# Optimization experiments

Measured on AMD Instinct MI355X. Metric: run time of the kernel, lower is better.

Reference implementation:

```python
import jax, jax.numpy as jnp
import numpy as np

B, L, V, E, H, DH, M, NL, BS, NR = 4, 2048, 32000, 512, 8, 64, 2048, 4, 64, 3
NEG = -1e9


def _sinusoidal_pe(length, dim):
    # LRA common_layers sinusoidal init: first half sin, second half cos.
    pos = np.arange(length, dtype=np.float32)[:, None]
    half = dim // 2
    div = np.exp(np.arange(half, dtype=np.float32) * -(np.log(10000.0) / half))
    pe = np.zeros((length, dim), np.float32)
    pe[:, :half] = np.sin(pos * div)
    pe[:, half:2 * half] = np.cos(pos * div)
    return jnp.asarray(pe)


def _bigbird_block_mask(seq_len, block_size, num_rand, seed):
    # BigBird sparsity at block granularity: window(3-band) + global(first/last
    # block rows & cols) + num_rand random blocks per row (connectivity_seed).
    nb = seq_len // block_size
    m = np.zeros((nb, nb), dtype=bool)
    for i in range(nb):
        for d in (-1, 0, 1):
            j = i + d
            if 0 <= j < nb:
                m[i, j] = True
    m[0, :] = True
    m[-1, :] = True
    m[:, 0] = True
    m[:, -1] = True
    rng = np.random.RandomState(seed)
    for i in range(1, nb - 1):
        avoid = {0, nb - 1, i - 1, i, i + 1}
        cand = np.array([j for j in range(nb) if j not in avoid])
        pick = rng.permutation(cand)[:num_rand]
        m[i, pick] = True
    return jnp.asarray(np.kron(m, np.ones((block_size, block_size), dtype=bool)))


_SPARSE_MASKS = [_bigbird_block_mask(L, BS, NR, lyr) for lyr in range(NL)]  # [L,L] bool per layer
_PE = _sinusoidal_pe(L, E)


def _ln(x, scale, bias, eps=1e-6):
    mu = jnp.mean(x, axis=-1, keepdims=True)
    var = jnp.mean(jnp.square(x - mu), axis=-1, keepdims=True)
    return (x - mu) * jax.lax.rsqrt(var + eps) * scale + bias


def setup_inputs() -> dict:
    key = jax.random.key(0)
    ks = jax.random.split(key, 12)
    s_qkv = 1.0 / np.sqrt(E)
    s_mlp = 1.0 / np.sqrt(E)
    return {
        "tokens": jax.random.randint(ks[0], (B, L), 0, V, dtype=jnp.int32),
        "embed": jax.random.normal(ks[1], (V, E), jnp.float32),
        "ln1_s": jnp.ones((NL, E), jnp.float32),
        "ln1_b": jnp.zeros((NL, E), jnp.float32),
        "wq": jax.random.normal(ks[2], (NL, E, H, DH), jnp.float32) * s_qkv,
        "wk": jax.random.normal(ks[3], (NL, E, H, DH), jnp.float32) * s_qkv,
        "wv": jax.random.normal(ks[4], (NL, E, H, DH), jnp.float32) * s_qkv,
        "wo": jax.random.normal(ks[5], (NL, H, DH, E), jnp.float32) * s_qkv,
        "ln2_s": jnp.ones((NL, E), jnp.float32),
        "ln2_b": jnp.zeros((NL, E), jnp.float32),
        "w1": jax.random.normal(ks[6], (NL, E, M), jnp.float32) * s_mlp,
        "b1": jnp.zeros((NL, M), jnp.float32),
        "w2": jax.random.normal(ks[7], (NL, M, E), jnp.float32) * (1.0 / np.sqrt(M)),
        "b2": jnp.zeros((NL, E), jnp.float32),
        "lnf_s": jnp.ones((E,), jnp.float32),
        "lnf_b": jnp.zeros((E,), jnp.float32),
    }


def reference(tokens, embed, ln1_s, ln1_b, wq, wk, wv, wo,
              ln2_s, ln2_b, w1, b1, w2, b2, lnf_s, lnf_b):
    pad = tokens > 0                                  # [B,L]
    x = embed[tokens] + _PE[None]                     # [B,L,E]
    scale = 1.0 / jnp.sqrt(jnp.asarray(DH, x.dtype))
    for lyr in range(NL):
        y = _ln(x, ln1_s[lyr], ln1_b[lyr])
        q = jnp.einsum("ble,ehd->blhd", y, wq[lyr]) * scale
        k = jnp.einsum("ble,ehd->blhd", y, wk[lyr])
        v = jnp.einsum("ble,ehd->blhd", y, wv[lyr])
        scores = jnp.einsum("blhd,bmhd->bhlm", q, k)  # [B,H,L,L]
        mask = (_SPARSE_MASKS[lyr][None, None]
                & pad[:, None, :, None] & pad[:, None, None, :])
        probs = jax.nn.softmax(jnp.where(mask, scores, NEG), axis=-1)
        o = jnp.einsum("bhlm,bmhd->blhd", probs, v)
        x = x + jnp.einsum("blhd,hde->ble", o, wo[lyr])
        y = _ln(x, ln2_s[lyr], ln2_b[lyr])
        h = jax.nn.gelu(jnp.einsum("ble,em->blm", y, w1[lyr]) + b1[lyr])
        x = x + jnp.einsum("blm,me->ble", h, w2[lyr]) + b2[lyr]
    return _ln(x, lnf_s, lnf_b)
```

## Files before the change

kernel.cpp:

```cpp
#include <hip/hip_runtime.h>
#include <hip/hip_bf16.h>
#include <cmath>
#include <cstdint>
#include <cstddef>

#define B_   4
#define L_   2048
#define E_   512
#define H_   8
#define DH_  64
#define M_   2048
#define NL_  4
#define NB_  32
#define BS_  64
#define CH_  12

typedef short bf16x8 __attribute__((ext_vector_type(8)));
typedef short bf16x4 __attribute__((ext_vector_type(4)));
typedef float f32x4 __attribute__((ext_vector_type(4)));

__device__ __forceinline__ short f2bf(float f) {
    union { __hip_bfloat16 h; short s; } u;
    u.h = __float2bfloat16(f);
    return u.s;
}
__device__ __forceinline__ float bf2f(short s) {
    union { short s; __hip_bfloat16 h; } u;
    u.s = s;
    return __bfloat162float(u.h);
}

struct MaskTable { unsigned m[NL_][NB_]; };
struct CxMT { unsigned key[624]; int pos; };

constexpr unsigned cx_next(CxMT& st) {
    if (st.pos >= 624) {
        for (int i = 0; i < 624; ++i) {
            unsigned y = (st.key[i] & 0x80000000u) | (st.key[(i + 1) % 624] & 0x7fffffffu);
            st.key[i] = st.key[(i + 397) % 624] ^ (y >> 1) ^ ((y & 1u) ? 0x9908b0dfu : 0u);
        }
        st.pos = 0;
    }
    unsigned y = st.key[st.pos++];
    y ^= y >> 11;
    y ^= (y << 7) & 0x9d2c5680u;
    y ^= (y << 15) & 0xefc60000u;
    y ^= y >> 18;
    return y;
}
constexpr unsigned cx_interval(CxMT& st, unsigned maxv) {
    if (maxv == 0u) return 0u;
    unsigned mask = maxv;
    mask |= mask >> 1; mask |= mask >> 2; mask |= mask >> 4;
    mask |= mask >> 8; mask |= mask >> 16;
    unsigned v = cx_next(st) & mask;
    while (v > maxv) v = cx_next(st) & mask;
    return v;
}
constexpr MaskTable compute_masks() {
    MaskTable T{};
    for (int lyr = 0; lyr < NL_; ++lyr) {
        unsigned m[NB_] = {};
        for (int i = 0; i < NB_; ++i) {
            unsigned w = 1u << i;
            if (i > 0) w |= 1u << (i - 1);
            if (i < NB_ - 1) w |= 1u << (i + 1);
            w |= 1u | (1u << (NB_ - 1));
            m[i] = w;
        }
        m[0] = 0xffffffffu;
        m[NB_ - 1] = 0xffffffffu;
        CxMT st{};
        unsigned s = (unsigned)lyr;
        for (int i = 0; i < 624; ++i) {
            st.key[i] = s;
            s = 1812433253u * (s ^ (s >> 30)) + (unsigned)i + 1u;
        }
        st.pos = 624;
        for (int i = 1; i < NB_ - 1; ++i) {
            int cand[NB_] = {};
            int n = 0;
            for (int j = 0; j < NB_; ++j) {
                if (j == 0 || j == NB_ - 1 || j == i - 1 || j == i || j == i + 1) continue;
                cand[n++] = j;
            }
            for (int kk = n - 1; kk >= 1; --kk) {
                int jj = (int)cx_interval(st, (unsigned)kk);
                int tmp = cand[kk]; cand[kk] = cand[jj]; cand[jj] = tmp;
            }
            m[i] |= (1u << cand[0]) | (1u << cand[1]) | (1u << cand[2]);
        }
        for (int i = 0; i < NB_; ++i) T.m[lyr][i] = m[i];
    }
    return T;
}

struct WorkTable {
    int n_items[NL_];
    int n_cmb[NL_];
    unsigned char itm_qb[NL_][40];
    unsigned char itm_j0[NL_][40];
    unsigned char itm_jn[NL_][40];
    unsigned char itm_slot[NL_][40];
    unsigned char cmb_qb[NL_][8];
    unsigned char cmb_slot0[NL_][8];
    unsigned char cmb_nch[NL_][8];
    unsigned char jlist[NL_][NB_][NB_];
};

constexpr WorkTable compute_work() {
    WorkTable T{};
    MaskTable M = compute_masks();
    for (int lyr = 0; lyr < NL_; ++lyr) {
        int items = 0, slots = 0, ncmb = 0;
        for (int qb = 0; qb < NB_; ++qb) {
            int cnt = 0;
            for (int j = 0; j < NB_; ++j)
                if ((M.m[lyr][qb] >> j) & 1u)
                    T.jlist[lyr][qb][cnt++] = (unsigned char)j;
            int nch = (cnt + CH_ - 1) / CH_;
            if (nch == 1) {
                T.itm_qb[lyr][items] = (unsigned char)qb;
                T.itm_j0[lyr][items] = 0;
                T.itm_jn[lyr][items] = (unsigned char)cnt;
                T.itm_slot[lyr][items] = 0xFF;
                items++;
            } else {
                T.cmb_qb[lyr][ncmb] = (unsigned char)qb;
                T.cmb_slot0[lyr][ncmb] = (unsigned char)slots;
                T.cmb_nch[lyr][ncmb] = (unsigned char)nch;
                ncmb++;
                int base = cnt / nch, rem = cnt % nch, off = 0;
                for (int c = 0; c < nch; ++c) {
                    int cl = base + (c < rem ? 1 : 0);
                    T.itm_qb[lyr][items] = (unsigned char)qb;
                    T.itm_j0[lyr][items] = (unsigned char)off;
                    T.itm_jn[lyr][items] = (unsigned char)cl;
                    T.itm_slot[lyr][items] = (unsigned char)slots;
                    items++; slots++; off += cl;
                }
            }
        }
        T.n_items[lyr] = items;
        T.n_cmb[lyr] = ncmb;
    }
    return T;
}

static constexpr WorkTable WT_HOST = compute_work();
__constant__ WorkTable g_wt = compute_work();

__global__ __launch_bounds__(256) void embed_kernel(const int* __restrict__ tokens,
                                                    const float* __restrict__ embed,
                                                    float* __restrict__ x) {
    int idx = blockIdx.x * 256 + threadIdx.x;
    int l = idx >> 6;
    int e0 = (idx & 63) * 8;
    float pe[8];
    #pragma unroll
    for (int j = 0; j < 8; ++j) {
        int e = e0 + j;
        int jj = e & 255;
        float div = expf((float)jj * -0.03597789207717895f);
        float arg = (float)l * div;
        pe[j] = (e < 256) ? sinf(arg) : cosf(arg);
    }
    #pragma unroll
    for (int b = 0; b < B_; ++b) {
        int tok = tokens[b * L_ + l];
        const float* em = embed + (size_t)tok * E_ + e0;
        f32x4 v0 = *(const f32x4*)em;
        f32x4 v1 = *(const f32x4*)(em + 4);
        #pragma unroll
        for (int j = 0; j < 4; ++j) { v0[j] += pe[j]; v1[j] += pe[4 + j]; }
        float* xo = x + ((size_t)(b * L_ + l)) * E_ + e0;
        *(f32x4*)xo = v0;
        *(f32x4*)(xo + 4) = v1;
    }
}

template<int OUTBF>
__global__ __launch_bounds__(256) void ln_kernel(const float* __restrict__ x,
                                                 const float* __restrict__ gamma,
                                                 const float* __restrict__ beta,
                                                 void* __restrict__ yout) {
    int t = threadIdx.x;
    int lane = t & 63;
    int row = blockIdx.x * 4 + (t >> 6);
    const float* xr = x + (size_t)row * E_ + lane * 8;
    f32x4 a0 = *(const f32x4*)xr;
    f32x4 a1 = *(const f32x4*)(xr + 4);
    float s = a0[0] + a0[1] + a0[2] + a0[3] + a1[0] + a1[1] + a1[2] + a1[3];
    #pragma unroll
    for (int off = 1; off < 64; off <<= 1) s += __shfl_xor(s, off, 64);
    float mu = s * (1.0f / E_);
    float q = 0.0f;
    #pragma unroll
    for (int j = 0; j < 4; ++j) { float d = a0[j] - mu; q += d * d; }
    #pragma unroll
    for (int j = 0; j < 4; ++j) { float d = a1[j] - mu; q += d * d; }
    #pragma unroll
    for (int off = 1; off < 64; off <<= 1) q += __shfl_xor(q, off, 64);
    float rstd = rsqrtf(q * (1.0f / E_) + 1e-6f);
    f32x4 g0 = *(const f32x4*)(gamma + lane * 8);
    f32x4 g1 = *(const f32x4*)(gamma + lane * 8 + 4);
    f32x4 b0 = *(const f32x4*)(beta + lane * 8);
    f32x4 b1 = *(const f32x4*)(beta + lane * 8 + 4);
    float o[8];
    #pragma unroll
    for (int j = 0; j < 4; ++j) o[j] = (a0[j] - mu) * rstd * g0[j] + b0[j];
    #pragma unroll
    for (int j = 0; j < 4; ++j) o[4 + j] = (a1[j] - mu) * rstd * g1[j] + b1[j];
    if (OUTBF) {
        bf16x8 pk;
        #pragma unroll
        for (int j = 0; j < 8; ++j) pk[j] = f2bf(o[j]);
        *(bf16x8*)((short*)yout + (size_t)row * E_ + lane * 8) = pk;
    } else {
        float* yr = (float*)yout + (size_t)row * E_ + lane * 8;
        *(f32x4*)yr = f32x4{o[0], o[1], o[2], o[3]};
        *(f32x4*)(yr + 4) = f32x4{o[4], o[5], o[6], o[7]};
    }
}

__global__ __launch_bounds__(256) void convT_kernel(const float* __restrict__ W,
                                                    short* __restrict__ Wt,
                                                    int K, int N,
                                                    size_t wStride, size_t wtStride,
                                                    float scale) {
    __shared__ float Ts[64][65];
    const float* Wl = W + blockIdx.z * wStride;
    short* Wtl = Wt + blockIdx.z * wtStride;
    int n0 = blockIdx.x * 64, k0 = blockIdx.y * 64;
    int t = threadIdx.x;
    int c = t & 63, r0 = t >> 6;
    #pragma unroll
    for (int i = 0; i < 16; ++i) {
        int r = r0 * 16 + i;
        Ts[r][c] = Wl[(size_t)(k0 + r) * N + n0 + c] * scale;
    }
    __syncthreads();
    #pragma unroll
    for (int i = 0; i < 16; ++i) {
        int r = r0 * 16 + i;
        Wtl[(size_t)(n0 + r) * K + k0 + c] = f2bf(Ts[c][r]);
    }
}

__device__ __forceinline__ float gelu_tanh(float x) {
    float u = x * (1.5957691216057308f + 0.07135480122394604f * x * x);
    return x / (1.0f + __expf(-u));
}

template<int BM, int BN, int WR, int WC, int ACT, int OUTBF>
__global__ __launch_bounds__(256) void mgemm_kernel(const short* __restrict__ A,
                                                    const short* __restrict__ Bt,
                                                    const float* __restrict__ bias,
                                                    const float* __restrict__ res,
                                                    void* __restrict__ Cout,
                                                    int M, int N, int K) {
    constexpr int FM = BM / WR / 16;
    constexpr int FN = BN / WC / 16;
    constexpr int ASZ = BM * 64;
    constexpr int BSZ = BN * 64;
    constexpr int PAD = 8;
    constexpr int CW = BN + PAD;
    static_assert((size_t)(OUTBF ? BM * CW * 2 : BM * CW * 4) <= (size_t)2 * (ASZ + BSZ) * 2,
                  "epilogue stage must fit in dbuf LDS");
    __shared__ __align__(16) short smem[2 * (ASZ + BSZ)];

    int t = threadIdx.x;
    int w = t >> 6, l = t & 63;
    int l15 = l & 15, lg = l >> 4;
    int wr = w / WC, wc = w % WC;
    int rowbase = wr * (BM / WR), colbase = wc * (BN / WC);
    int brow = blockIdx.y * BM, bcol = blockIdx.x * BN;
    int swz = ((l & 7) ^ (l >> 3)) * 8;
    int lrow = l >> 3;
    f32x4 acc[FM][FN] = {};

    const int nt = K >> 6;

    auto stage = [&](int buf, int k0) {
        short* Ad = smem + buf * ASZ;
        short* Bd = smem + 2 * ASZ + buf * BSZ;
        #pragma unroll
        for (int it = 0; it < BM / 32; ++it) {
            int row8 = (it * 4 + w) * 8;
            const short* ga = A + (size_t)(brow + row8 + lrow) * K + k0 + swz;
            __builtin_amdgcn_global_load_lds(
                (const __attribute__((address_space(1))) unsigned int*)ga,
                (__attribute__((address_space(3))) unsigned int*)(Ad + row8 * 64),
                16, 0, 0);
        }
        #pragma unroll
        for (int it = 0; it < BN / 32; ++it) {
            int row8 = (it * 4 + w) * 8;
            const short* gb = Bt + (size_t)(bcol + row8 + lrow) * K + k0 + swz;
            __builtin_amdgcn_global_load_lds(
                (const __attribute__((address_space(1))) unsigned int*)gb,
                (__attribute__((address_space(3))) unsigned int*)(Bd + row8 * 64),
                16, 0, 0);
        }
    };

    stage(0, 0);
    asm volatile("s_waitcnt vmcnt(0)" ::: "memory");
    __builtin_amdgcn_s_barrier();

    int cur = 0;
    for (int kt = 0; kt < nt; ++kt) {
        if (kt + 1 < nt) stage(cur ^ 1, (kt + 1) << 6);
        const short* Ar = smem + cur * ASZ;
        const short* Br = smem + 2 * ASZ + cur * BSZ;
        #pragma unroll
        for (int kk = 0; kk < 64; kk += 32) {
            bf16x8 af[FM], bfr[FN];
            #pragma unroll
            for (int m = 0; m < FM; ++m)
                af[m] = *(const bf16x8*)(Ar + (rowbase + m * 16 + l15) * 64
                                            + (((kk >> 3) + lg) ^ (l15 & 7)) * 8);
            #pragma unroll
            for (int n = 0; n < FN; ++n)
                bfr[n] = *(const bf16x8*)(Br + (colbase + n * 16 + l15) * 64
                                             + (((kk >> 3) + lg) ^ (l15 & 7)) * 8);
            #pragma unroll
            for (int m = 0; m < FM; ++m)
                #pragma unroll
                for (int n = 0; n < FN; ++n)
                    acc[m][n] = __builtin_amdgcn_mfma_f32_16x16x32_bf16(af[m], bfr[n], acc[m][n], 0, 0, 0);
        }
        asm volatile("s_waitcnt vmcnt(0) lgkmcnt(0)" ::: "memory");
        __builtin_amdgcn_s_barrier();
        cur ^= 1;
    }

    if (OUTBF) {
        short* Cs = smem;
        #pragma unroll
        for (int m = 0; m < FM; ++m) {
            int row = rowbase + m * 16 + lg * 4;
            #pragma unroll
            for (int n = 0; n < FN; ++n) {
                int col = colbase + n * 16 + l15;
                float bv = bias ? bias[bcol + col] : 0.0f;
                #pragma unroll
                for (int r = 0; r < 4; ++r) {
                    float vv = acc[m][n][r] + bv;
                    if (ACT == 1) vv = gelu_tanh(vv);
                    Cs[(row + r) * CW + col] = f2bf(vv);
                }
            }
        }
        __syncthreads();
        #pragma unroll
        for (int it = 0; it < BM * BN / 8 / 256; ++it) {
            int c = it * 256 + t;
            int row = c / (BN / 8), c8 = c % (BN / 8);
            *(bf16x8*)((short*)Cout + (size_t)(brow + row) * N + bcol + c8 * 8) =
                *(const bf16x8*)(Cs + row * CW + c8 * 8);
        }
    } else {
        float* Cs = (float*)smem;
        #pragma unroll
        for (int m = 0; m < FM; ++m) {
            int row = rowbase + m * 16 + lg * 4;
            #pragma unroll
            for (int n = 0; n < FN; ++n) {
                int col = colbase + n * 16 + l15;
                float bv = bias ? bias[bcol + col] : 0.0f;
                #pragma unroll
                for (int r = 0; r < 4; ++r)
                    Cs[(row + r) * CW + col] = acc[m][n][r] + bv;
            }
        }
        __syncthreads();
        #pragma unroll
        for (int it = 0; it < BM * BN / 4 / 256; ++it) {
            int c = it * 256 + t;
            int row = c / (BN / 4), c4 = c % (BN / 4);
            f32x4 vv = *(const f32x4*)(Cs + row * CW + c4 * 4);
            size_t gi = (size_t)(brow + row) * N + bcol + c4 * 4;
            if (res) vv += *(const f32x4*)(res + gi);
            *(f32x4*)((float*)Cout + gi) = vv;
        }
    }
}

#define KSTR 72

__global__ __launch_bounds__(256) void attn_kernel(const short* __restrict__ qkv,
                                                   const int* __restrict__ tokens,
                                                   short* __restrict__ o,
                                                   float* __restrict__ pacc,
                                                   float* __restrict__ pm,
                                                   float* __restrict__ pl,
                                                   int lyr) {
    __shared__ __align__(16) short Ks[64][KSTR];
    __shared__ __align__(16) short Vt[64][KSTR];
    __shared__ __align__(16) short Pw[4][16][KSTR];
    __shared__ unsigned long long qbits_s;
    __shared__ unsigned long long kbits_s;

    int item = blockIdx.x, h = blockIdx.y, b = blockIdx.z;
    int qb   = g_wt.itm_qb[lyr][item];
    int j0   = g_wt.itm_j0[lyr][item];
    int jn   = g_wt.itm_jn[lyr][item];
    int slot = g_wt.itm_slot[lyr][item];
    const unsigned char* jl = g_wt.jlist[lyr][qb];

    int t = threadIdx.x;
    int l = t & 63, w = t >> 6;
    int l15 = l & 15, lg = l >> 4;
    int srow = t >> 3, sdb = t & 7;

    if (t < 64) {
        unsigned long long qm = __ballot(tokens[b * L_ + qb * 64 + t] > 0);
        if (t == 0) qbits_s = qm;
    }

    int qrow = qb * 64 + w * 16 + l15;
    const short* qp = qkv + (size_t)(b * L_ + qrow) * 1536 + h * 64;
    bf16x8 qf0 = *(const bf16x8*)(qp + lg * 8);
    bf16x8 qf1 = *(const bf16x8*)(qp + lg * 8 + 32);

    f32x4 acc[4] = {};
    float m_r = -INFINITY, l_r = 0.0f;

    bf16x8 kr0, kr1, vr0, vr1;
    int pn = 0;
    auto LOAD = [&](int ci) {
        int jb = jl[j0 + ci];
        const short* base = qkv + (size_t)(b * L_ + jb * 64 + srow) * 1536 + h * 64;
        kr0 = *(const bf16x8*)(base + 512 + sdb * 8);
        kr1 = *(const bf16x8*)(base + (size_t)32 * 1536 + 512 + sdb * 8);
        vr0 = *(const bf16x8*)(base + 1024 + sdb * 8);
        vr1 = *(const bf16x8*)(base + (size_t)32 * 1536 + 1024 + sdb * 8);
        if (t < 64) pn = tokens[b * L_ + jb * 64 + t];
    };
    LOAD(0);

    for (int ci = 0; ci < jn; ++ci) {
        __syncthreads();
        *(bf16x8*)&Ks[srow][sdb * 8] = kr0;
        *(bf16x8*)&Ks[srow + 32][sdb * 8] = kr1;
        #pragma unroll
        for (int j = 0; j < 8; ++j) {
            Vt[sdb * 8 + j][(srow & 7) + 8 * ((srow >> 3) ^ sdb)] = vr0[j];
            Vt[sdb * 8 + j][(srow & 7) + 8 * (((srow >> 3) + 4) ^ sdb)] = vr1[j];
        }
        if (t < 64) {
            unsigned long long km = __ballot(pn > 0);
            if (t == 0) kbits_s = km;
        }
        __syncthreads();

        if (ci + 1 < jn) LOAD(ci + 1);

        f32x4 sacc[4];
        __builtin_amdgcn_s_setprio(1);
        #pragma unroll
        for (int f = 0; f < 4; ++f) {
            bf16x8 kk0 = *(const bf16x8*)&Ks[16 * f + l15][lg * 8];
            bf16x8 kk1 = *(const bf16x8*)&Ks[16 * f + l15][lg * 8 + 32];
            f32x4 z = {};
            z = __builtin_amdgcn_mfma_f32_16x16x32_bf16(kk0, qf0, z, 0, 0, 0);
            z = __builtin_amdgcn_mfma_f32_16x16x32_bf16(kk1, qf1, z, 0, 0, 0);
            sacc[f] = z;
        }
        __builtin_amdgcn_s_setprio(0);

        unsigned long long kb = kbits_s;
        bool pq = (qbits_s >> (w * 16 + l15)) & 1ull;
        unsigned vm = 0;
        #pragma unroll
        for (int f = 0; f < 4; ++f)
            vm |= ((unsigned)(kb >> (16 * f + 4 * lg)) & 0xFu) << (4 * f);
        if (!pq) vm = 0;

        float mx = -INFINITY;
        #pragma unroll
        for (int f = 0; f < 4; ++f)
            #pragma unroll
            for (int r = 0; r < 4; ++r)
                if ((vm >> (4 * f + r)) & 1u) mx = fmaxf(mx, sacc[f][r]);
        mx = fmaxf(mx, __shfl_xor(mx, 16, 64));
        mx = fmaxf(mx, __shfl_xor(mx, 32, 64));
        float nm = fmaxf(m_r, mx);

        float pv[16];
        float sum = 0.0f;
        #pragma unroll
        for (int f = 0; f < 4; ++f)
            #pragma unroll
            for (int r = 0; r < 4; ++r) {
                float p = ((vm >> (4 * f + r)) & 1u) ? __expf(sacc[f][r] - nm) : 0.0f;
                pv[4 * f + r] = p;
                sum += p;
            }
        sum += __shfl_xor(sum, 16, 64);
        sum += __shfl_xor(sum, 32, 64);
        float al = (nm == -INFINITY) ? 1.0f : __expf(m_r - nm);
        m_r = nm;
        l_r = l_r * al + sum;

        #pragma unroll
        for (int f = 0; f < 4; ++f) {
            bf16x4 pk;
            #pragma unroll
            for (int r = 0; r < 4; ++r) pk[r] = f2bf(pv[4 * f + r]);
            *(bf16x4*)&Pw[w][l15][16 * f + 4 * lg] = pk;
        }

        float alr[4];
        #pragma unroll
        for (int r = 0; r < 4; ++r) alr[r] = __shfl(al, lg * 4 + r, 64);
        #pragma unroll
        for (int fd = 0; fd < 4; ++fd)
            #pragma unroll
            for (int r = 0; r < 4; ++r) acc[fd][r] *= alr[r];

        bf16x8 pa0 = *(const bf16x8*)&Pw[w][l15][lg * 8];
        bf16x8 pa1 = *(const bf16x8*)&Pw[w][l15][lg * 8 + 32];
        __builtin_amdgcn_s_setprio(1);
        #pragma unroll
        for (int fd = 0; fd < 4; ++fd) {
            int dd = 16 * fd + l15;
            bf16x8 vv0 = *(const bf16x8*)&Vt[dd][8 * (lg ^ (dd >> 3))];
            bf16x8 vv1 = *(const bf16x8*)&Vt[dd][8 * ((4 + lg) ^ (dd >> 3))];
            acc[fd] = __builtin_amdgcn_mfma_f32_16x16x32_bf16(pa0, vv0, acc[fd], 0, 0, 0);
            acc[fd] = __builtin_amdgcn_mfma_f32_16x16x32_bf16(pa1, vv1, acc[fd], 0, 0, 0);
        }
        __builtin_amdgcn_s_setprio(0);
    }

    float lrr[4], mrr[4];
    #pragma unroll
    for (int r = 0; r < 4; ++r) {
        lrr[r] = __shfl(l_r, lg * 4 + r, 64);
        mrr[r] = __shfl(m_r, lg * 4 + r, 64);
    }
    unsigned long long qbits = qbits_s;

    if (slot == 0xFF) {
        #pragma unroll
        for (int r = 0; r < 4; ++r) {
            int rw = lg * 4 + r;
            int gl = qb * 64 + w * 16 + rw;
            size_t ob = (size_t)(b * L_ + gl) * 512 + h * 64 + l15;
            bool ok = ((qbits >> (w * 16 + rw)) & 1ull) && (lrr[r] > 0.0f);
            if (ok) {
                float inv = 1.0f / lrr[r];
                #pragma unroll
                for (int fd = 0; fd < 4; ++fd) o[ob + 16 * fd] = f2bf(acc[fd][r] * inv);
            } else {
                #pragma unroll
                for (int fd = 0; fd < 4; ++fd) {
                    float s = 0.0f;
                    for (int m = 0; m < L_; ++m)
                        s += bf2f(qkv[(size_t)(b * L_ + m) * 1536 + 1024 + h * 64 + 16 * fd + l15]);
                    o[ob + 16 * fd] = f2bf(s * (1.0f / L_));
                }
            }
        }
    } else {
        size_t pb = ((size_t)slot * B_ + b) * H_ + h;
        #pragma unroll
        for (int r = 0; r < 4; ++r) {
            int rloc = w * 16 + lg * 4 + r;
            #pragma unroll
            for (int fd = 0; fd < 4; ++fd)
                pacc[pb * 4096 + (size_t)rloc * 64 + 16 * fd + l15] = acc[fd][r];
            if (l15 == 0) {
                pm[pb * 64 + rloc] = mrr[r];
                pl[pb * 64 + rloc] = lrr[r];
            }
        }
    }
}

__global__ __launch_bounds__(256) void attn_combine(const short* __restrict__ qkv,
                                                    const int* __restrict__ tokens,
                                                    short* __restrict__ o,
                                                    const float* __restrict__ pacc,
                                                    const float* __restrict__ pm,
                                                    const float* __restrict__ pl,
                                                    int lyr) {
    int ci = blockIdx.x, h = blockIdx.y, b = blockIdx.z;
    int qb  = g_wt.cmb_qb[lyr][ci];
    int s0  = g_wt.cmb_slot0[lyr][ci];
    int nch = g_wt.cmb_nch[lyr][ci];
    int t = threadIdx.x;
    int r = t >> 2, dq = t & 3;
    int grow = qb * 64 + r;
    bool pq = tokens[b * L_ + grow] > 0;
    float M = -INFINITY;
    for (int c = 0; c < nch; ++c)
        M = fmaxf(M, pm[(((size_t)(s0 + c) * B_ + b) * H_ + h) * 64 + r]);
    size_t ob = (size_t)(b * L_ + grow) * 512 + h * 64 + dq * 16;
    if (pq && M > -1e30f) {
        float lsum = 0.0f;
        float accd[16] = {};
        for (int c = 0; c < nch; ++c) {
            size_t pb = ((size_t)(s0 + c) * B_ + b) * H_ + h;
            float wgt = __expf(pm[pb * 64 + r] - M);
            lsum += pl[pb * 64 + r] * wgt;
            const float* pa = pacc + pb * 4096 + (size_t)r * 64 + dq * 16;
            #pragma unroll
            for (int j = 0; j < 16; ++j) accd[j] += pa[j] * wgt;
        }
        float inv = 1.0f / lsum;
        #pragma unroll
        for (int j = 0; j < 16; ++j) o[ob + j] = f2bf(accd[j] * inv);
    } else {
        #pragma unroll
        for (int j = 0; j < 16; ++j) {
            float s = 0.0f;
            for (int m = 0; m < L_; ++m)
                s += bf2f(qkv[(size_t)(b * L_ + m) * 1536 + 1024 + h * 64 + dq * 16 + j]);
            o[ob + j] = f2bf(s * (1.0f / L_));
        }
    }
}

extern "C" void kernel_launch(void* const* d_in, const int* in_sizes, int n_in,
                              void* d_out, int out_size, void* d_ws, size_t ws_size,
                              hipStream_t stream) {
    (void)in_sizes; (void)n_in; (void)out_size; (void)ws_size;
    const int*   tokens = (const int*)d_in[0];
    const float* embed  = (const float*)d_in[1];
    const float* ln1_s  = (const float*)d_in[2];
    const float* ln1_b  = (const float*)d_in[3];
    const float* wq     = (const float*)d_in[4];
    const float* wk     = (const float*)d_in[5];
    const float* wv     = (const float*)d_in[6];
    const float* wo     = (const float*)d_in[7];
    const float* ln2_s  = (const float*)d_in[8];
    const float* ln2_b  = (const float*)d_in[9];
    const float* w1     = (const float*)d_in[10];
    const float* b1     = (const float*)d_in[11];
    const float* w2     = (const float*)d_in[12];
    const float* b2     = (const float*)d_in[13];
    const float* lnf_s  = (const float*)d_in[14];
    const float* lnf_b  = (const float*)d_in[15];
    float* out = (float*)d_out;

    const size_t BLE = (size_t)B_ * L_ * E_;
    char* ws = (char*)d_ws;
    float* x    = (float*)ws;
    short* yb   = (short*)(x + BLE);
    short* R    = yb + BLE;
    short* qkv  = R;
    short* ob   = R + 3 * BLE;
    short* hb   = R;
    short* qkvt = R + 4 * BLE;
    short* wot  = qkvt + (size_t)NL_ * 1536 * 512;
    short* w1t  = wot + (size_t)NL_ * 512 * 512;
    short* w2t  = w1t + (size_t)NL_ * 2048 * 512;
    float* pacc = (float*)(w2t + (size_t)NL_ * 512 * 2048);
    float* pm   = pacc + (size_t)8 * B_ * H_ * 4096;
    float* pl   = pm + (size_t)8 * B_ * H_ * 64;

    convT_kernel<<<dim3(8, 8, NL_), 256, 0, stream>>>(wq, qkvt,          512, 512, 262144, 786432, 0.125f);
    convT_kernel<<<dim3(8, 8, NL_), 256, 0, stream>>>(wk, qkvt + 262144, 512, 512, 262144, 786432, 1.0f);
    convT_kernel<<<dim3(8, 8, NL_), 256, 0, stream>>>(wv, qkvt + 524288, 512, 512, 262144, 786432, 1.0f);
    convT_kernel<<<dim3(8, 8, NL_), 256, 0, stream>>>(wo, wot,           512, 512, 262144, 262144, 1.0f);
    convT_kernel<<<dim3(32, 8, NL_), 256, 0, stream>>>(w1, w1t,          512, 2048, 1048576, 1048576, 1.0f);
    convT_kernel<<<dim3(8, 32, NL_), 256, 0, stream>>>(w2, w2t,          2048, 512, 1048576, 1048576, 1.0f);

    embed_kernel<<<(L_ * E_ / 8) / 256, 256, 0, stream>>>(tokens, embed, x);

    const int MR = B_ * L_;
    const int LNG = MR / 4;
    for (int lyr = 0; lyr < NL_; ++lyr) {
        ln_kernel<1><<<LNG, 256, 0, stream>>>(x, ln1_s + lyr * E_, ln1_b + lyr * E_, yb);
        mgemm_kernel<128, 128, 2, 2, 0, 1><<<dim3(12, 64), 256, 0, stream>>>(
            yb, qkvt + (size_t)lyr * 786432, nullptr, nullptr, qkv, MR, 1536, 512);
        attn_kernel<<<dim3(WT_HOST.n_items[lyr], H_, B_), 256, 0, stream>>>(
            qkv, tokens, ob, pacc, pm, pl, lyr);
        attn_combine<<<dim3(WT_HOST.n_cmb[lyr], H_, B_), 256, 0, stream>>>(
            qkv, tokens, ob, pacc, pm, pl, lyr);
        mgemm_kernel<64, 128, 2, 2, 0, 0><<<dim3(4, 128), 256, 0, stream>>>(
            ob, wot + (size_t)lyr * 262144, nullptr, x, x, MR, 512, 512);
        ln_kernel<1><<<LNG, 256, 0, stream>>>(x, ln2_s + lyr * E_, ln2_b + lyr * E_, yb);
        mgemm_kernel<128, 128, 2, 2, 1, 1><<<dim3(16, 64), 256, 0, stream>>>(
            yb, w1t + (size_t)lyr * 1048576, b1 + (size_t)lyr * M_, nullptr, hb, MR, 2048, 512);
        mgemm_kernel<64, 128, 2, 2, 0, 0><<<dim3(4, 128), 256, 0, stream>>>(
            hb, w2t + (size_t)lyr * 1048576, b2 + (size_t)lyr * E_, x, x, MR, 512, 2048);
    }
    ln_kernel<0><<<LNG, 256, 0, stream>>>(x, lnf_s, lnf_b, out);
}
```

Baseline: 684.9 us.

## Use 512-thread GEMM blocks with 2x4 warps and XCD-aware block remapping

The GEMM kernel now runs 8 wavefronts per workgroup in a 2x4 layout, so each wave holds fewer accumulator fragments. The staging and epilogue loops are rewritten for 512 threads. Workgroup IDs are also remapped so that consecutive tiles land on the same XCD (chiplet), which is meant to improve L2 reuse of shared A/B tiles. The trade-off is more threads per block for the same LDS footprint, which lowers per-wave work and may affect occupancy. The remap assumes the grid size is divisible by 8.

```diff
diff --git a/kernel.cpp b/kernel.cpp
--- a/kernel.cpp
+++ b/kernel.cpp
@@ -252,13 +252,14 @@
     return x / (1.0f + __expf(-u));
 }
 
-template<int BM, int BN, int WR, int WC, int ACT, int OUTBF>
-__global__ __launch_bounds__(256) void mgemm_kernel(const short* __restrict__ A,
+template<int BM, int BN, int ACT, int OUTBF>
+__global__ __launch_bounds__(512) void mgemm_kernel(const short* __restrict__ A,
                                                     const short* __restrict__ Bt,
                                                     const float* __restrict__ bias,
                                                     const float* __restrict__ res,
                                                     void* __restrict__ Cout,
                                                     int M, int N, int K) {
+    constexpr int WR = 2, WC = 4;
     constexpr int FM = BM / WR / 16;
     constexpr int FN = BN / WC / 16;
     constexpr int ASZ = BM * 64;
@@ -272,11 +273,16 @@
     int t = threadIdx.x;
     int w = t >> 6, l = t & 63;
     int l15 = l & 15, lg = l >> 4;
-    int wr = w / WC, wc = w % WC;
+    int wr = w >> 2, wc = w & 3;
     int rowbase = wr * (BM / WR), colbase = wc * (BN / WC);
-    int brow = blockIdx.y * BM, bcol = blockIdx.x * BN;
-    int swz = ((l & 7) ^ (l >> 3)) * 8;
-    int lrow = l >> 3;
+
+    int nwg = (int)(gridDim.x * gridDim.y);
+    int orig = (int)(blockIdx.y * gridDim.x + blockIdx.x);
+    int sid = (orig & 7) * (nwg >> 3) + (orig >> 3);
+    int bx = sid % (int)gridDim.x, by = sid / (int)gridDim.x;
+    int brow = by * BM, bcol = bx * BN;
+
+    int swz = ((t & 7) ^ ((t >> 3) & 7)) * 8;
     f32x4 acc[FM][FN] = {};
 
     const int nt = K >> 6;
@@ -285,21 +291,21 @@
         short* Ad = smem + buf * ASZ;
         short* Bd = smem + 2 * ASZ + buf * BSZ;
         #pragma unroll
-        for (int it = 0; it < BM / 32; ++it) {
-            int row8 = (it * 4 + w) * 8;
-            const short* ga = A + (size_t)(brow + row8 + lrow) * K + k0 + swz;
+        for (int it = 0; it < BM / 64; ++it) {
+            int row = it * 64 + (t >> 3);
+            const short* ga = A + (size_t)(brow + row) * K + k0 + swz;
             __builtin_amdgcn_global_load_lds(
                 (const __attribute__((address_space(1))) unsigned int*)ga,
-                (__attribute__((address_space(3))) unsigned int*)(Ad + row8 * 64),
+                (__attribute__((address_space(3))) unsigned int*)(Ad + (it * 64 + w * 8) * 64),
                 16, 0, 0);
         }
         #pragma unroll
-        for (int it = 0; it < BN / 32; ++it) {
-            int row8 = (it * 4 + w) * 8;
-            const short* gb = Bt + (size_t)(bcol + row8 + lrow) * K + k0 + swz;
+        for (int it = 0; it < BN / 64; ++it) {
+            int row = it * 64 + (t >> 3);
+            const short* gb = Bt + (size_t)(bcol + row) * K + k0 + swz;
             __builtin_amdgcn_global_load_lds(
                 (const __attribute__((address_space(1))) unsigned int*)gb,
-                (__attribute__((address_space(3))) unsigned int*)(Bd + row8 * 64),
+                (__attribute__((address_space(3))) unsigned int*)(Bd + (it * 64 + w * 8) * 64),
                 16, 0, 0);
         }
     };
@@ -354,8 +360,8 @@
         }
         __syncthreads();
         #pragma unroll
-        for (int it = 0; it < BM * BN / 8 / 256; ++it) {
-            int c = it * 256 + t;
+        for (int it = 0; it < BM * BN / 8 / 512; ++it) {
+            int c = it * 512 + t;
             int row = c / (BN / 8), c8 = c % (BN / 8);
             *(bf16x8*)((short*)Cout + (size_t)(brow + row) * N + bcol + c8 * 8) =
                 *(const bf16x8*)(Cs + row * CW + c8 * 8);
@@ -376,8 +382,8 @@
         }
         __syncthreads();
         #pragma unroll
-        for (int it = 0; it < BM * BN / 4 / 256; ++it) {
-            int c = it * 256 + t;
+        for (int it = 0; it < BM * BN / 4 / 512; ++it) {
+            int c = it * 512 + t;
             int row = c / (BN / 4), c4 = c % (BN / 4);
             f32x4 vv = *(const f32x4*)(Cs + row * CW + c4 * 4);
             size_t gi = (size_t)(brow + row) * N + bcol + c4 * 4;
@@ -674,18 +680,18 @@
     const int LNG = MR / 4;
     for (int lyr = 0; lyr < NL_; ++lyr) {
         ln_kernel<1><<<LNG, 256, 0, stream>>>(x, ln1_s + lyr * E_, ln1_b + lyr * E_, yb);
-        mgemm_kernel<128, 128, 2, 2, 0, 1><<<dim3(12, 64), 256, 0, stream>>>(
+        mgemm_kernel<128, 128, 0, 1><<<dim3(12, 64), 512, 0, stream>>>(
             yb, qkvt + (size_t)lyr * 786432, nullptr, nullptr, qkv, MR, 1536, 512);
         attn_kernel<<<dim3(WT_HOST.n_items[lyr], H_, B_), 256, 0, stream>>>(
             qkv, tokens, ob, pacc, pm, pl, lyr);
         attn_combine<<<dim3(WT_HOST.n_cmb[lyr], H_, B_), 256, 0, stream>>>(
             qkv, tokens, ob, pacc, pm, pl, lyr);
-        mgemm_kernel<64, 128, 2, 2, 0, 0><<<dim3(4, 128), 256, 0, stream>>>(
+        mgemm_kernel<64, 128, 0, 0><<<dim3(4, 128), 512, 0, stream>>>(
             ob, wot + (size_t)lyr * 262144, nullptr, x, x, MR, 512, 512);
         ln_kernel<1><<<LNG, 256, 0, stream>>>(x, ln2_s + lyr * E_, ln2_b + lyr * E_, yb);
-        mgemm_kernel<128, 128, 2, 2, 1, 1><<<dim3(16, 64), 256, 0, stream>>>(
+        mgemm_kernel<128, 128, 1, 1><<<dim3(16, 64), 512, 0, stream>>>(
             yb, w1t + (size_t)lyr * 1048576, b1 + (size_t)lyr * M_, nullptr, hb, MR, 2048, 512);
-        mgemm_kernel<64, 128, 2, 2, 0, 0><<<dim3(4, 128), 256, 0, stream>>>(
+        mgemm_kernel<64, 128, 0, 0><<<dim3(4, 128), 512, 0, stream>>>(
             hb, w2t + (size_t)lyr * 1048576, b2 + (size_t)lyr * E_, x, x, MR, 512, 2048);
     }
     ln_kernel<0><<<LNG, 256, 0, stream>>>(x, lnf_s, lnf_b, out);
```

Result: faster. 602.3 us (-12.1%).
